# Kernel optimization log

Hardware: AMD Instinct MI355X
Metric: run time of the kernel (lower is better)

## Reference

```python
import jax, jax.numpy as jnp
import numpy as np

KERNEL_MUL = 2.0
KERNEL_NUM = 5


def setup_inputs() -> dict:
    key = jax.random.key(0)
    k1, k2 = jax.random.split(key)
    source = jax.random.normal(k1, (4096, 1024), dtype=jnp.float32)
    target = jax.random.normal(k2, (4096, 1024), dtype=jnp.float32)
    return {"source": source, "target": target}


def reference(source, target):
    bs = source.shape[0]
    total = jnp.concatenate([source, target], axis=0)  # [n, D]
    n = total.shape[0]
    # Pairwise squared L2 distances via the GEMM trick: ||a-b||^2 = a^2 + b^2 - 2ab
    sq = jnp.sum(total * total, axis=1)                 # [n]
    L2 = sq[:, None] + sq[None, :] - 2.0 * (total @ total.T)  # [n, n]
    # Bandwidth computed from detached distances (torch used .data => stop_gradient)
    bw = jax.lax.stop_gradient(L2).sum() / (n * n - n)
    bw = bw / (KERNEL_MUL ** (KERNEL_NUM // 2))
    bws = bw * (KERNEL_MUL ** jnp.arange(KERNEL_NUM, dtype=L2.dtype))  # [K]
    # Multi-bandwidth Gaussian kernel sum: [K, n, n] -> [n, n]
    K = jnp.exp(-L2[None, :, :] / bws[:, None, None]).sum(axis=0)
    XX = K[:bs, :bs].mean()
    YY = K[bs:, bs:].mean()
    XY = K[:bs, bs:].mean()
    YX = K[bs:, :bs].mean()
    return XX + YY - XY - YX
```

## Files before the change

kernel.cpp:

```cpp
#include <hip/hip_runtime.h>
#include <hip/hip_bf16.h>
#include <stdint.h>
#include <stddef.h>

#define NTOT 8192
#define BS   4096
#define DIM  1024
#define NTRI 2080
#define QS   20.0f

#define OFF_TB      0u
#define OFF_SQ      8388608u
#define OFF_COLPART 8421376u
#define OFF_COLP2   10518528u
#define OFF_BWP     10551296u
#define OFF_PART    10551360u


typedef __attribute__((ext_vector_type(4)))  int   i32x4;
typedef __attribute__((ext_vector_type(16))) int   i32x16;

__device__ __forceinline__ float fast_sqrt(float x) {
#if __has_builtin(__builtin_amdgcn_sqrtf)
  return __builtin_amdgcn_sqrtf(x);
#else
  float r; asm("v_sqrt_f32 %0, %1" : "=v"(r) : "v"(x)); return r;
#endif
}

__device__ __forceinline__ float fast_exp2(float x) {
#if __has_builtin(__builtin_amdgcn_exp2f)
  return __builtin_amdgcn_exp2f(x);
#else
  float r; asm("v_exp_f32 %0, %1" : "=v"(r) : "v"(x)); return r;
#endif
}

__device__ __forceinline__ void load_lds16(const void* g, void* l) {
  __builtin_amdgcn_global_load_lds((const __attribute__((address_space(1))) void*)g,
                                   (__attribute__((address_space(3))) void*)l,
                                   16, 0, 0);
}

__device__ __forceinline__ int quant4(float4 v) {
  int q0 = __float2int_rn(fminf(fmaxf(v.x * QS, -127.f), 127.f));
  int q1 = __float2int_rn(fminf(fmaxf(v.y * QS, -127.f), 127.f));
  int q2 = __float2int_rn(fminf(fmaxf(v.z * QS, -127.f), 127.f));
  int q3 = __float2int_rn(fminf(fmaxf(v.w * QS, -127.f), 127.f));
  return (q0 & 255) | ((q1 & 255) << 8) | ((q2 & 255) << 16) | ((q3 & 255) << 24);
}

__global__ __launch_bounds__(256) void prep_kernel(const float* __restrict__ src,
                                                   const float* __restrict__ tgt,
                                                   unsigned char* __restrict__ tb,
                                                   float* __restrict__ sq,
                                                   float* __restrict__ colpart) {
  const int t = threadIdx.x;
  const int lane = t & 63, wave = t >> 6;
  const int R = blockIdx.x;
  const int r0 = R * 16;
  const int kt = t >> 4, kq = (t >> 2) & 3, b0 = (t & 3) * 4;
  unsigned char* dstbase = tb + (size_t)R * 16384 + kt * 1024 + kq * 256 + b0;
  __shared__ float rs[16][4];
  float c0 = 0.f, c1 = 0.f, c2 = 0.f, c3 = 0.f;
#pragma unroll 4
  for (int r = 0; r < 16; ++r) {
    const int row = r0 + r;
    const float* base = (row < BS) ? (src + (size_t)row * DIM)
                                   : (tgt + (size_t)(row - BS) * DIM);
    float4 v = *reinterpret_cast<const float4*>(base + t * 4);
    *reinterpret_cast<int*>(dstbase + r * 16) = quant4(v);
    c0 += v.x; c1 += v.y; c2 += v.z; c3 += v.w;
    float s = v.x*v.x + v.y*v.y + v.z*v.z + v.w*v.w;
#pragma unroll
    for (int off = 32; off > 0; off >>= 1) s += __shfl_down(s, off, 64);
    if (lane == 0) rs[r][wave] = s;
  }
  float4 cp = {c0, c1, c2, c3};
  *reinterpret_cast<float4*>(colpart + (size_t)R * 1024 + t * 4) = cp;
  __syncthreads();
  if (t < 16) sq[r0 + t] = (rs[t][0] + rs[t][1]) + (rs[t][2] + rs[t][3]);
}

__global__ __launch_bounds__(1024) void colred_kernel(const float* __restrict__ colpart,
                                                      float* __restrict__ colp2) {
  const int b = blockIdx.x, t = threadIdx.x;
  float s = 0.f;
  for (int g = b * 64; g < b * 64 + 64; ++g) s += colpart[(size_t)g * 1024 + t];
  colp2[b * 1024 + t] = s;
}

__global__ __launch_bounds__(1024) void bw_kernel(const float* __restrict__ sq,
                                                  const float* __restrict__ colp2,
                                                  float* __restrict__ bwp) {
  const int t = threadIdx.x;
  double s1 = 0.0;
#pragma unroll
  for (int i = 0; i < 8; ++i) s1 += (double)sq[t + i * 1024];
  float s = 0.f;
#pragma unroll
  for (int j = 0; j < 8; ++j) s += colp2[j * 1024 + t];
  double s2 = (double)s * (double)s;
  __shared__ double r1[1024], r2[1024];
  r1[t] = s1; r2[t] = s2;
  __syncthreads();
  for (int off = 512; off > 0; off >>= 1) {
    if (t < off) { r1[t] += r1[t + off]; r2[t] += r2[t + off]; }
    __syncthreads();
  }
  if (t == 0) {
    const double n = (double)NTOT;
    double sumL2 = 2.0 * n * r1[0] - 2.0 * r2[0];
    double bw = sumL2 / (n * n - n);
    bw = bw / 4.0;
    const double LOG2E = 1.4426950408889634;
    for (int k = 0; k < 5; ++k)
      bwp[k] = (float)(-LOG2E / (bw * (double)(1 << k)));
  }
}

#define STAGE(kt1024, ldsA, ldsB)                                             \
  do {                                                                        \
    load_lds16(T + a0g + (kt1024), (ldsA) + (size_t)(wave * 64) * 16);        \
    load_lds16(T + a1g + (kt1024), (ldsA) + (size_t)(256 + wave * 64) * 16);  \
    load_lds16(T + b0g + (kt1024), (ldsB) + (size_t)(wave * 64) * 16);        \
    load_lds16(T + b1g + (kt1024), (ldsB) + (size_t)(256 + wave * 64) * 16);  \
  } while (0)

#define COMPUTE64(Abuf, Bbuf)                                                 \
  do {                                                                        \
    _Pragma("unroll")                                                         \
    for (int kk = 0; kk < 2; ++kk) {                                          \
      i32x4 fa0 = *reinterpret_cast<const i32x4*>(&(Abuf)[abase + kk * 512]); \
      i32x4 fa1 = *reinterpret_cast<const i32x4*>(&(Abuf)[abase + 2048 + kk * 512]); \
      i32x4 fb0 = *reinterpret_cast<const i32x4*>(&(Bbuf)[bbase + kk * 512]); \
      i32x4 fb1 = *reinterpret_cast<const i32x4*>(&(Bbuf)[bbase + 2048 + kk * 512]); \
      acc00 = __builtin_amdgcn_mfma_i32_32x32x32_i8(fa0, fb0, acc00, 0, 0, 0); \
      acc01 = __builtin_amdgcn_mfma_i32_32x32x32_i8(fa0, fb1, acc01, 0, 0, 0); \
      acc10 = __builtin_amdgcn_mfma_i32_32x32x32_i8(fa1, fb0, acc10, 0, 0, 0); \
      acc11 = __builtin_amdgcn_mfma_i32_32x32x32_i8(fa1, fb1, acc11, 0, 0, 0); \
    }                                                                         \
  } while (0)

#define BARR __builtin_amdgcn_s_barrier()

#define EXP5(x16) ({ float u_ = fast_exp2(x16);                               \
                     float u2_ = u_ * u_, u4_ = u2_ * u2_;                    \
                     float u8_ = u4_ * u4_, u16_ = u8_ * u8_;                 \
                     ((u_ + u2_) + (u4_ + u8_)) + u16_; })

__global__ __launch_bounds__(256, 4) void mmd_gemm(const unsigned char* __restrict__ T,
                                                   const float* __restrict__ sq,
                                                   const float* __restrict__ bwp,
                                                   float* __restrict__ partials) {
  __shared__ __align__(16) unsigned char sA0[8192], sA1[8192];
  __shared__ __align__(16) unsigned char sB0[8192], sB1[8192];
  __shared__ float wred[4];

  const int tid  = threadIdx.x;
  const int lane = tid & 63;
  const int wave = tid >> 6;
  const int wr   = wave >> 1;
  const int wc   = wave & 1;

  const int tno = (blockIdx.x & 7) * 260 + (blockIdx.x >> 3);
  int bi = (int)((129.0f - fast_sqrt(129.0f * 129.0f - 8.0f * (float)tno)) * 0.5f);
  while (bi > 0 && bi * (129 - bi) / 2 > tno) --bi;
  while ((bi + 1) * (129 - (bi + 1)) / 2 <= tno) ++bi;
  const int bj = bi + (tno - bi * (129 - bi) / 2);

  const int aRB = bi * 8, bRB = bj * 8;

  const int f0 = tid, f1 = 256 + tid;
  const size_t a0g = (size_t)(aRB + (f0 >> 6)) * 16384 + (f0 & 63) * 16;
  const size_t a1g = (size_t)(aRB + (f1 >> 6)) * 16384 + (f1 & 63) * 16;
  const size_t b0g = (size_t)(bRB + (f0 >> 6)) * 16384 + (f0 & 63) * 16;
  const size_t b1g = (size_t)(bRB + (f1 >> 6)) * 16384 + (f1 & 63) * 16;

  i32x16 acc00 = {}, acc01 = {}, acc10 = {}, acc11 = {};

  const int col5 = lane & 31;
  const int hi32 = lane >> 5;
  const int abase = (wr * 4 + (col5 >> 4)) * 1024 + hi32 * 256 + (lane & 15) * 16;
  const int bbase = (wc * 4 + (col5 >> 4)) * 1024 + hi32 * 256 + (lane & 15) * 16;

  STAGE(0, sA0, sB0);

  for (int t = 0; t < 8; ++t) {
    STAGE((2 * t + 1) * 1024, sA1, sB1);
    asm volatile("s_waitcnt vmcnt(4)" ::: "memory");
    BARR;
    __builtin_amdgcn_sched_barrier(0);
    COMPUTE64(sA0, sB0);
    __builtin_amdgcn_sched_barrier(0);
    BARR;

    if (t < 7) {
      STAGE((2 * t + 2) * 1024, sA0, sB0);
      asm volatile("s_waitcnt vmcnt(4)" ::: "memory");
    } else {
      asm volatile("s_waitcnt vmcnt(0)" ::: "memory");
    }
    BARR;
    __builtin_amdgcn_sched_barrier(0);
    COMPUTE64(sA1, sB1);
    __builtin_amdgcn_sched_barrier(0);
    BARR;
  }

  const float s16 = bwp[0] * 0.0625f;
  const float c2i = -2.f * s16 / (QS * QS);

  const float bj0 = sq[bj * 128 + wc * 64 + col5] * s16;
  const float bj1 = sq[bj * 128 + wc * 64 + 32 + col5] * s16;

  float tsum = 0.f;
#pragma unroll
  for (int tm = 0; tm < 2; ++tm) {
    const int rbaseq = bi * 128 + wr * 64 + tm * 32 + 4 * hi32;
#pragma unroll
    for (int q = 0; q < 4; ++q) {
#pragma unroll
      for (int p = 0; p < 4; ++p) {
        const float ai = sq[rbaseq + q * 8 + p] * s16;
        const int r = q * 4 + p;
        const int v0 = tm ? acc10[r] : acc00[r];
        const int v1 = tm ? acc11[r] : acc01[r];
        tsum += EXP5(fmaf((float)v0, c2i, ai + bj0));
        tsum += EXP5(fmaf((float)v1, c2i, ai + bj1));
      }
    }
  }

#pragma unroll
  for (int off = 32; off > 0; off >>= 1) tsum += __shfl_down(tsum, off, 64);
  if (lane == 0) wred[wave] = tsum;
  __syncthreads();
  if (tid == 0) {
    float sign = ((bi < 32) == (bj < 32)) ? 1.f : -1.f;
    float wgt  = (bi == bj) ? 1.f : 2.f;
    partials[tno] = sign * wgt * ((wred[0] + wred[1]) + (wred[2] + wred[3]));
  }
}

__global__ __launch_bounds__(256) void finish_kernel(const float* __restrict__ partials,
                                                     float* __restrict__ out) {
  const int t = threadIdx.x;
  double s = 0.0;
  for (int i = t; i < NTRI; i += 256) s += (double)partials[i];
  __shared__ double rd[256];
  rd[t] = s;
  __syncthreads();
  for (int off = 128; off > 0; off >>= 1) {
    if (t < off) rd[t] += rd[t + off];
    __syncthreads();
  }
  if (t == 0) out[0] = (float)(rd[0] / 16777216.0);
}

extern "C" void kernel_launch(void* const* d_in, const int* in_sizes, int n_in,
                              void* d_out, int out_size, void* d_ws, size_t ws_size,
                              hipStream_t stream) {
  const float* src = (const float*)d_in[0];
  const float* tgt = (const float*)d_in[1];
  char* ws = (char*)d_ws;
  unsigned char* tb = (unsigned char*)(ws + OFF_TB);
  float* sq       = (float*)(ws + OFF_SQ);
  float* colpart  = (float*)(ws + OFF_COLPART);
  float* colp2    = (float*)(ws + OFF_COLP2);
  float* bwp      = (float*)(ws + OFF_BWP);
  float* partials = (float*)(ws + OFF_PART);

  prep_kernel<<<dim3(512), dim3(256), 0, stream>>>(src, tgt, tb, sq, colpart);
  colred_kernel<<<dim3(8), dim3(1024), 0, stream>>>(colpart, colp2);
  bw_kernel<<<dim3(1), dim3(1024), 0, stream>>>(sq, colp2, bwp);
  mmd_gemm<<<dim3(NTRI), dim3(256), 0, stream>>>(tb, sq, bwp, partials);
  finish_kernel<<<dim3(1), dim3(256), 0, stream>>>(partials, (float*)d_out);
}
```

Before: 74.60 us.

## Load int8 MFMA fragments directly from global memory, dropping LDS staging

The int8 GEMM main loop no longer stages tiles through double-buffered LDS with barriers. Each wave now loads its MFMA operand fragments straight from global memory into registers, using a two-deep register prefetch. Launch bounds drop to 2 blocks per CU to leave room for the extra registers. This removes LDS traffic and barrier stalls, but each tile is now re-fetched by the waves that share it instead of loaded once per block, which puts more pressure on L1/L2 and can lower occupancy.

After: 82.93 us. 11.2% more time.

```diff
diff --git a/kernel.cpp b/kernel.cpp
--- a/kernel.cpp
+++ b/kernel.cpp
@@ -34,12 +34,6 @@
 #else
   float r; asm("v_exp_f32 %0, %1" : "=v"(r) : "v"(x)); return r;
 #endif
-}
-
-__device__ __forceinline__ void load_lds16(const void* g, void* l) {
-  __builtin_amdgcn_global_load_lds((const __attribute__((address_space(1))) void*)g,
-                                   (__attribute__((address_space(3))) void*)l,
-                                   16, 0, 0);
 }
 
 __device__ __forceinline__ int quant4(float4 v) {
@@ -119,42 +113,18 @@
   }
 }
 
-#define STAGE(kt1024, ldsA, ldsB)                                             \
-  do {                                                                        \
-    load_lds16(T + a0g + (kt1024), (ldsA) + (size_t)(wave * 64) * 16);        \
-    load_lds16(T + a1g + (kt1024), (ldsA) + (size_t)(256 + wave * 64) * 16);  \
-    load_lds16(T + b0g + (kt1024), (ldsB) + (size_t)(wave * 64) * 16);        \
-    load_lds16(T + b1g + (kt1024), (ldsB) + (size_t)(256 + wave * 64) * 16);  \
-  } while (0)
-
-#define COMPUTE64(Abuf, Bbuf)                                                 \
-  do {                                                                        \
-    _Pragma("unroll")                                                         \
-    for (int kk = 0; kk < 2; ++kk) {                                          \
-      i32x4 fa0 = *reinterpret_cast<const i32x4*>(&(Abuf)[abase + kk * 512]); \
-      i32x4 fa1 = *reinterpret_cast<const i32x4*>(&(Abuf)[abase + 2048 + kk * 512]); \
-      i32x4 fb0 = *reinterpret_cast<const i32x4*>(&(Bbuf)[bbase + kk * 512]); \
-      i32x4 fb1 = *reinterpret_cast<const i32x4*>(&(Bbuf)[bbase + 2048 + kk * 512]); \
-      acc00 = __builtin_amdgcn_mfma_i32_32x32x32_i8(fa0, fb0, acc00, 0, 0, 0); \
-      acc01 = __builtin_amdgcn_mfma_i32_32x32x32_i8(fa0, fb1, acc01, 0, 0, 0); \
-      acc10 = __builtin_amdgcn_mfma_i32_32x32x32_i8(fa1, fb0, acc10, 0, 0, 0); \
-      acc11 = __builtin_amdgcn_mfma_i32_32x32x32_i8(fa1, fb1, acc11, 0, 0, 0); \
-    }                                                                         \
-  } while (0)
-
-#define BARR __builtin_amdgcn_s_barrier()
+#define MFI8(a, b, c) __builtin_amdgcn_mfma_i32_32x32x32_i8(a, b, c, 0, 0, 0)
+#define LDQ(P, off) (*reinterpret_cast<const i32x4*>((P) + (off)))
 
 #define EXP5(x16) ({ float u_ = fast_exp2(x16);                               \
                      float u2_ = u_ * u_, u4_ = u2_ * u2_;                    \
                      float u8_ = u4_ * u4_, u16_ = u8_ * u8_;                 \
                      ((u_ + u2_) + (u4_ + u8_)) + u16_; })
 
-__global__ __launch_bounds__(256, 4) void mmd_gemm(const unsigned char* __restrict__ T,
+__global__ __launch_bounds__(256, 2) void mmd_gemm(const unsigned char* __restrict__ T,
                                                    const float* __restrict__ sq,
                                                    const float* __restrict__ bwp,
                                                    float* __restrict__ partials) {
-  __shared__ __align__(16) unsigned char sA0[8192], sA1[8192];
-  __shared__ __align__(16) unsigned char sB0[8192], sB1[8192];
   __shared__ float wred[4];
 
   const int tid  = threadIdx.x;
@@ -169,43 +139,35 @@
   while ((bi + 1) * (129 - (bi + 1)) / 2 <= tno) ++bi;
   const int bj = bi + (tno - bi * (129 - bi) / 2);
 
-  const int aRB = bi * 8, bRB = bj * 8;
-
-  const int f0 = tid, f1 = 256 + tid;
-  const size_t a0g = (size_t)(aRB + (f0 >> 6)) * 16384 + (f0 & 63) * 16;
-  const size_t a1g = (size_t)(aRB + (f1 >> 6)) * 16384 + (f1 & 63) * 16;
-  const size_t b0g = (size_t)(bRB + (f0 >> 6)) * 16384 + (f0 & 63) * 16;
-  const size_t b1g = (size_t)(bRB + (f1 >> 6)) * 16384 + (f1 & 63) * 16;
-
-  i32x16 acc00 = {}, acc01 = {}, acc10 = {}, acc11 = {};
-
   const int col5 = lane & 31;
   const int hi32 = lane >> 5;
-  const int abase = (wr * 4 + (col5 >> 4)) * 1024 + hi32 * 256 + (lane & 15) * 16;
-  const int bbase = (wc * 4 + (col5 >> 4)) * 1024 + hi32 * 256 + (lane & 15) * 16;
-
-  STAGE(0, sA0, sB0);
-
-  for (int t = 0; t < 8; ++t) {
-    STAGE((2 * t + 1) * 1024, sA1, sB1);
-    asm volatile("s_waitcnt vmcnt(4)" ::: "memory");
-    BARR;
-    __builtin_amdgcn_sched_barrier(0);
-    COMPUTE64(sA0, sB0);
-    __builtin_amdgcn_sched_barrier(0);
-    BARR;
-
-    if (t < 7) {
-      STAGE((2 * t + 2) * 1024, sA0, sB0);
-      asm volatile("s_waitcnt vmcnt(4)" ::: "memory");
-    } else {
-      asm volatile("s_waitcnt vmcnt(0)" ::: "memory");
+  const int lb   = hi32 * 256 + (lane & 15) * 16;
+
+  const unsigned char* Ap = T + (size_t)(bi * 8 + wr * 4 + (col5 >> 4)) * 16384 + lb;
+  const unsigned char* Bp = T + (size_t)(bj * 8 + wc * 4 + (col5 >> 4)) * 16384 + lb;
+
+  i32x16 acc00 = {}, acc01 = {}, acc10 = {}, acc11 = {};
+
+  i32x4 xa0 = LDQ(Ap, 0), xa1 = LDQ(Ap, 32768);
+  i32x4 xb0 = LDQ(Bp, 0), xb1 = LDQ(Bp, 32768);
+#pragma unroll
+  for (int s = 0; s < 32; s += 2) {
+    const int o1 = (s + 1) * 512;
+    i32x4 ya0 = LDQ(Ap, o1), ya1 = LDQ(Ap, 32768 + o1);
+    i32x4 yb0 = LDQ(Bp, o1), yb1 = LDQ(Bp, 32768 + o1);
+    acc00 = MFI8(xa0, xb0, acc00);
+    acc01 = MFI8(xa0, xb1, acc01);
+    acc10 = MFI8(xa1, xb0, acc10);
+    acc11 = MFI8(xa1, xb1, acc11);
+    if (s + 2 < 32) {
+      const int o2 = (s + 2) * 512;
+      xa0 = LDQ(Ap, o2); xa1 = LDQ(Ap, 32768 + o2);
+      xb0 = LDQ(Bp, o2); xb1 = LDQ(Bp, 32768 + o2);
     }
-    BARR;
-    __builtin_amdgcn_sched_barrier(0);
-    COMPUTE64(sA1, sB1);
-    __builtin_amdgcn_sched_barrier(0);
-    BARR;
+    acc00 = MFI8(ya0, yb0, acc00);
+    acc01 = MFI8(ya0, yb1, acc01);
+    acc10 = MFI8(ya1, yb0, acc10);
+    acc11 = MFI8(ya1, yb1, acc11);
   }
 
   const float s16 = bwp[0] * 0.0625f;
```
